# Kernel tuning notes

Measured on AMD Instinct MI355X. Metric: run time of the kernel, lower is better.

The kernel has to match this reference:

```python
import jax, jax.numpy as jnp
import numpy as np

G = 2        # num_code_vector_groups
V = 320      # num_code_vectors_per_group
D1 = 512     # extracted_feature_size
DCV = 768    # code_vector_size
DG = DCV // G  # per-group code vector dim = 384
TAU = 2.0    # gumbel_init_temperature
B, L = 16, 2048


def setup_inputs() -> dict:
    key = jax.random.key(0)
    k1, k2, k3, k4 = jax.random.split(key, 4)
    hidden_states = jax.random.normal(k1, (B, L, D1), dtype=jnp.float32)
    W = jax.random.normal(k2, (G * V, D1), dtype=jnp.float32) * 0.02
    b = jnp.zeros((G * V,), dtype=jnp.float32)
    code_book = jax.random.normal(k3, (1, G, V, DG), dtype=jnp.float32)
    # fixed Gumbel noise (torch samples it inside F.gumbel_softmax)
    gumbel_noise = jax.random.gumbel(k4, (B * L * G, V), dtype=jnp.float32)
    return {"hidden_states": hidden_states, "W": W, "b": b,
            "code_book": code_book, "gumbel_noise": gumbel_noise}


def reference(hidden_states, W, b, code_book, gumbel_noise):
    batch, length, _ = hidden_states.shape
    # linear projection: (B, L, G*V)
    logits = jnp.einsum('bld,od->blo', hidden_states, W) + b
    flat = logits.reshape(batch * length * G, V)  # (N*G, V)

    # gumbel_softmax(hard=True): straight-through hard one-hot
    y_soft = jax.nn.softmax((flat + gumbel_noise) / TAU, axis=-1)
    idx = jnp.argmax(y_soft, axis=-1)
    y_hard = jax.nn.one_hot(idx, V, dtype=y_soft.dtype)
    probs = y_hard + y_soft - jax.lax.stop_gradient(y_soft)  # (N*G, V)

    # redundant second softmax for perplexity (faithful to source)
    soft_dist = jax.nn.softmax(logits.reshape(batch, length, G, V), axis=-1)
    perplexity = soft_dist.sum(0) / batch  # (L, G, V) — sum over dim 0 only

    # code_vectors: (probs.unsqueeze(-1) * code_book).sum(-2) as an einsum
    p = probs.reshape(batch * length, G, V)
    code_vectors = jnp.einsum('ngv,gvd->ngd', p, code_book[0])
    code_vectors = code_vectors.reshape(batch, length, G * DG)  # (B, L, 768)
    return code_vectors, perplexity
```

## Files before the change

kernel.cpp:

```cpp
#include <hip/hip_runtime.h>

#define B_    16
#define L_    2048
#define D1_   512
#define G_    2
#define V_    320
#define GV_   640
#define DG_   384
#define NROW_ 32768
#define OUT0_ ((size_t)B_ * L_ * G_ * DG_)
#define WS_BYTES_ ((size_t)GV_ * D1_ * 2u)
#define WSA_OFF_SH_ ((size_t)GV_ * D1_)
#define LG_OFF_SH_  (WSA_OFF_SH_ + (size_t)NROW_ * D1_)
#define SPLIT2_WS_  ((LG_OFF_SH_ + (size_t)NROW_ * GV_) * 2u)
#define THR_  2e-2f
#define GPAD_ 324

typedef __attribute__((ext_vector_type(8))) short          s16x8;
typedef __attribute__((ext_vector_type(4))) float          f32x4;
typedef __attribute__((ext_vector_type(4))) int            s32x4;
typedef __attribute__((ext_vector_type(4))) unsigned short u16x4;

__device__ __forceinline__ unsigned short f2bf(float x) {
    unsigned u = __float_as_uint(x);
    u += 0x7fffu + ((u >> 16) & 1u);
    return (unsigned short)(u >> 16);
}
__device__ __forceinline__ float bf2f(unsigned short h) {
    return __uint_as_float(((unsigned)h) << 16);
}
__device__ __forceinline__ unsigned cvtpk(float lo, float hi) {
    unsigned r;
    asm("v_cvt_pk_bf16_f32 %0, %1, %2" : "=v"(r) : "v"(lo), "v"(hi));
    return r;
}
union PU { unsigned u[4]; s16x8 v; };
__device__ __forceinline__ s16x8 pack8(const float4& a, const float4& b) {
    PU p;
    p.u[0] = cvtpk(a.x, a.y); p.u[1] = cvtpk(a.z, a.w);
    p.u[2] = cvtpk(b.x, b.y); p.u[3] = cvtpk(b.z, b.w);
    return p.v;
}
__device__ __forceinline__ void merge2(float& m1, int& i1, float& m2, int& i2,
                                       float om1, int oi1, float om2, int oi2) {
    if (om1 > m1 || (om1 == m1 && oi1 < i1)) {
        if (m1 > om2 || (m1 == om2 && i1 < oi2)) { m2 = m1; i2 = i1; }
        else                                     { m2 = om2; i2 = oi2; }
        m1 = om1; i1 = oi1;
    } else if (om1 > m2 || (om1 == m2 && oi1 < i2)) { m2 = om1; i2 = oi1; }
}

__global__ void prep_w_kernel(const float* __restrict__ W, unsigned short* __restrict__ ws) {
    int flat = blockIdx.x * 256 + threadIdx.x;
    int o  = flat >> 7;
    int j0 = (flat & 127) << 2;
    float4 v = *(const float4*)(W + (size_t)o * D1_ + j0);
    int ch = o >> 4, kk = j0 >> 5;
    int slot = (o & 15) + (((j0 >> 3) & 3) << 4);
    size_t off = (((size_t)(ch * 16 + kk) * 64 + slot) << 3) + (j0 & 7);
    ws[off + 0] = f2bf(v.x); ws[off + 1] = f2bf(v.y);
    ws[off + 2] = f2bf(v.z); ws[off + 3] = f2bf(v.w);
}

__global__ void prep_a_kernel(const float* __restrict__ hidden, unsigned short* __restrict__ wsA) {
    size_t flat = (size_t)blockIdx.x * 256 + threadIdx.x;
    int r  = (int)(flat >> 7);
    int j0 = ((int)flat & 127) << 2;
    float4 v = *(const float4*)(hidden + ((size_t)r << 9) + j0);
    int ch = r >> 4, kk = j0 >> 5;
    int slot = (r & 15) + (((j0 >> 3) & 3) << 4);
    size_t off = (((size_t)(ch * 16 + kk) * 64 + slot) << 3) + (j0 & 7);
    wsA[off + 0] = f2bf(v.x); wsA[off + 1] = f2bf(v.y);
    wsA[off + 2] = f2bf(v.z); wsA[off + 3] = f2bf(v.w);
}

__global__ __launch_bounds__(512, 4) void k1_gemm(
    const unsigned short* __restrict__ wsW,
    const unsigned short* __restrict__ wsA,
    const float* __restrict__ bias,
    unsigned short* __restrict__ lgout)
{
    const int tid = threadIdx.x;
    const int w = tid >> 6, lane = tid & 63;
    const int rg = w >> 1, cg = w & 1;
    const int q = lane >> 4, c = lane & 15;
    const int d = blockIdx.x;
    const int mt = (d & 7) * 32 + (d >> 5);
    const int ct = (d >> 3) & 3;

    const unsigned short* a0p = wsA + ((size_t)(mt * 8 + rg * 2 + 0) << 13) + (lane << 3);
    const unsigned short* a1p = wsA + ((size_t)(mt * 8 + rg * 2 + 1) << 13) + (lane << 3);
    const unsigned short* wp  = wsW + ((size_t)(ct * 10 + cg * 5) << 13) + (lane << 3);

    f32x4 acc0[5], acc1[5];
#pragma unroll
    for (int cf = 0; cf < 5; ++cf) { acc0[cf] = (f32x4){0,0,0,0}; acc1[cf] = (f32x4){0,0,0,0}; }

    s16x8 Aa0, Aa1, Aw0, Aw1, Aw2, Aw3, Aw4;
    s16x8 Ba0, Ba1, Bw0, Bw1, Bw2, Bw3, Bw4;

#define LD(S, KK) { \
        S##a0 = *(const s16x8*)(a0p + (KK) * 512); \
        S##a1 = *(const s16x8*)(a1p + (KK) * 512); \
        S##w0 = *(const s16x8*)(wp + 0 * 8192 + (KK) * 512); \
        S##w1 = *(const s16x8*)(wp + 1 * 8192 + (KK) * 512); \
        S##w2 = *(const s16x8*)(wp + 2 * 8192 + (KK) * 512); \
        S##w3 = *(const s16x8*)(wp + 3 * 8192 + (KK) * 512); \
        S##w4 = *(const s16x8*)(wp + 4 * 8192 + (KK) * 512); }
#define MM(S) { \
        acc0[0] = __builtin_amdgcn_mfma_f32_16x16x32_bf16(S##a0, S##w0, acc0[0], 0, 0, 0); \
        acc1[0] = __builtin_amdgcn_mfma_f32_16x16x32_bf16(S##a1, S##w0, acc1[0], 0, 0, 0); \
        acc0[1] = __builtin_amdgcn_mfma_f32_16x16x32_bf16(S##a0, S##w1, acc0[1], 0, 0, 0); \
        acc1[1] = __builtin_amdgcn_mfma_f32_16x16x32_bf16(S##a1, S##w1, acc1[1], 0, 0, 0); \
        acc0[2] = __builtin_amdgcn_mfma_f32_16x16x32_bf16(S##a0, S##w2, acc0[2], 0, 0, 0); \
        acc1[2] = __builtin_amdgcn_mfma_f32_16x16x32_bf16(S##a1, S##w2, acc1[2], 0, 0, 0); \
        acc0[3] = __builtin_amdgcn_mfma_f32_16x16x32_bf16(S##a0, S##w3, acc0[3], 0, 0, 0); \
        acc1[3] = __builtin_amdgcn_mfma_f32_16x16x32_bf16(S##a1, S##w3, acc1[3], 0, 0, 0); \
        acc0[4] = __builtin_amdgcn_mfma_f32_16x16x32_bf16(S##a0, S##w4, acc0[4], 0, 0, 0); \
        acc1[4] = __builtin_amdgcn_mfma_f32_16x16x32_bf16(S##a1, S##w4, acc1[4], 0, 0, 0); }

    LD(A, 0)
#pragma unroll 1
    for (int kp = 0; kp < 8; ++kp) {
        LD(B, 2 * kp + 1)
        MM(A)
        if (kp < 7) LD(A, 2 * kp + 2)
        MM(B)
    }
#undef LD
#undef MM

    float bv[5];
#pragma unroll
    for (int cf = 0; cf < 5; ++cf) bv[cf] = bias[ct * 160 + cg * 80 + cf * 16 + c];
#pragma unroll
    for (int rf = 0; rf < 2; ++rf) {
        size_t mrow = (size_t)mt * 128 + rg * 32 + rf * 16 + q * 4;
        unsigned short* op = lgout + mrow * GV_ + ct * 160 + cg * 80 + c;
        const f32x4* ac = rf ? acc1 : acc0;
#pragma unroll
        for (int cf = 0; cf < 5; ++cf)
#pragma unroll
            for (int r = 0; r < 4; ++r)
                op[(size_t)r * GV_ + cf * 16] = f2bf(ac[cf][r] + bv[cf]);
    }
}

__global__ __launch_bounds__(256, 4) void k2_epi(
    const float* __restrict__ hidden,
    const float* __restrict__ W,
    const float* __restrict__ bias,
    const float* __restrict__ cb,
    const float* __restrict__ gn,
    const unsigned short* __restrict__ lgb,
    float* __restrict__ out)
{
    __shared__ float PERPW[4][GV_];
    const int tid = threadIdx.x;
    const int w = tid >> 6, lane = tid & 63;
    const int h = lane >> 5, k = lane & 31;
    const int l = blockIdx.x;

    f32x4 pac0 = {0,0,0,0}, pac1 = {0,0,0,0}, pac2 = {0,0,0,0};

    f32x4 Alg0, Alg1, Alg2, Agv0, Agv1, Agv2;
    f32x4 Blg0, Blg1, Blg2, Bgv0, Bgv1, Bgv2;

#define NTL(p) __builtin_nontemporal_load((const f32x4*)(p))
#define LOADROW(S, RR) { \
        size_t row_ = ((size_t)(w * 4 + (RR))) * L_ + l; \
        const unsigned short* lrb = lgb + row_ * GV_ + h * V_ + (k << 2); \
        const float* grb = gn + row_ * GV_ + h * V_ + (k << 2); \
        u16x4 L0 = *(const u16x4*)(lrb); \
        u16x4 L1 = *(const u16x4*)(lrb + 128); \
        S##gv0 = NTL(grb); S##gv1 = NTL(grb + 128); \
        _Pragma("unroll") \
        for (int j = 0; j < 4; ++j) { S##lg0[j] = bf2f(L0[j]); S##lg1[j] = bf2f(L1[j]); } \
        if (k < 16) { \
            u16x4 L2 = *(const u16x4*)(lrb + 256); \
            S##gv2 = NTL(grb + 256); \
            _Pragma("unroll") \
            for (int j = 0; j < 4; ++j) S##lg2[j] = bf2f(L2[j]); \
        } }

#define EXACT(CI, EN) { \
        if (EN) { \
            const int ci_ = (CI); \
            const float* ar_ = hidden + row_ * D1_ + (k << 4); \
            const float* wr_ = W + (size_t)(h * V_ + ci_) * D1_ + (k << 4); \
            double s_ = 0.0; \
            _Pragma("unroll 4") \
            for (int j = 0; j < 16; ++j) s_ = fma((double)ar_[j], (double)wr_[j], s_); \
            _Pragma("unroll") \
            for (int off = 1; off <= 16; off <<= 1) s_ += __shfl_xor(s_, off); \
            s_ += (double)bias[h * V_ + ci_] + (double)gn[row_ * GV_ + h * V_ + ci_]; \
            if (s_ > bestv || (s_ == bestv && ci_ < bi)) { bestv = s_; bi = ci_; } \
        } }

#define PROCROW(S, RR) { \
        const size_t row_ = ((size_t)(w * 4 + (RR))) * L_ + l; \
         \
        _Pragma("unroll") \
        for (int j = 0; j < 4; ++j) { S##gv0[j] += S##lg0[j]; S##gv1[j] += S##lg1[j]; } \
        if (k < 16) { _Pragma("unroll") for (int j = 0; j < 4; ++j) S##gv2[j] += S##lg2[j]; } \
         \
        float m1 = -3e38f; \
        _Pragma("unroll") \
        for (int j = 0; j < 4; ++j) { m1 = fmaxf(m1, S##gv0[j]); m1 = fmaxf(m1, S##gv1[j]); } \
        if (k < 16) { _Pragma("unroll") for (int j = 0; j < 4; ++j) m1 = fmaxf(m1, S##gv2[j]); } \
        _Pragma("unroll") \
        for (int mk = 1; mk <= 16; mk <<= 1) m1 = fmaxf(m1, __shfl_xor(m1, mk)); \
         \
        int li = 0x7fffffff; \
        _Pragma("unroll") \
        for (int j = 0; j < 4; ++j) { \
            if (S##gv0[j] == m1) li = min(li, (k << 2) + j); \
            if (S##gv1[j] == m1) li = min(li, ((k + 32) << 2) + j); } \
        if (k < 16) { _Pragma("unroll") for (int j = 0; j < 4; ++j) if (S##gv2[j] == m1) li = min(li, ((k + 64) << 2) + j); } \
        _Pragma("unroll") \
        for (int mk = 1; mk <= 16; mk <<= 1) li = min(li, __shfl_xor(li, mk)); \
        const int i1 = li; \
         \
        float m2 = -3e38f; \
        _Pragma("unroll") \
        for (int j = 0; j < 4; ++j) { \
            if (((k << 2) + j) != i1)        m2 = fmaxf(m2, S##gv0[j]); \
            if ((((k + 32) << 2) + j) != i1) m2 = fmaxf(m2, S##gv1[j]); } \
        if (k < 16) { _Pragma("unroll") for (int j = 0; j < 4; ++j) if ((((k + 64) << 2) + j) != i1) m2 = fmaxf(m2, S##gv2[j]); } \
        _Pragma("unroll") \
        for (int mk = 1; mk <= 16; mk <<= 1) m2 = fmaxf(m2, __shfl_xor(m2, mk)); \
         \
        float se = 0.f; \
        _Pragma("unroll") \
        for (int j = 0; j < 4; ++j) { \
            S##lg0[j] = __expf(S##lg0[j]); se += S##lg0[j]; \
            S##lg1[j] = __expf(S##lg1[j]); se += S##lg1[j]; } \
        if (k < 16) { _Pragma("unroll") for (int j = 0; j < 4; ++j) { S##lg2[j] = __expf(S##lg2[j]); se += S##lg2[j]; } } \
        _Pragma("unroll") \
        for (int mk = 1; mk <= 16; mk <<= 1) se += __shfl_xor(se, mk); \
        const float inv = 1.0f / (se * 16.0f); \
        _Pragma("unroll") \
        for (int j = 0; j < 4; ++j) { pac0[j] += S##lg0[j] * inv; pac1[j] += S##lg1[j] * inv; } \
        if (k < 16) { _Pragma("unroll") for (int j = 0; j < 4; ++j) pac2[j] += S##lg2[j] * inv; } \
        int idx = i1; \
        if (m1 - m2 < THR_) { \
             \
            int li2 = 0x7fffffff; \
            _Pragma("unroll") \
            for (int j = 0; j < 4; ++j) { \
                int v0 = (k << 2) + j;        if (v0 != i1 && S##gv0[j] == m2) li2 = min(li2, v0); \
                int v1 = ((k + 32) << 2) + j; if (v1 != i1 && S##gv1[j] == m2) li2 = min(li2, v1); } \
            if (k < 16) { _Pragma("unroll") for (int j = 0; j < 4; ++j) { int v2 = ((k + 64) << 2) + j; if (v2 != i1 && S##gv2[j] == m2) li2 = min(li2, v2); } } \
            _Pragma("unroll") \
            for (int mk = 1; mk <= 16; mk <<= 1) li2 = min(li2, __shfl_xor(li2, mk)); \
            const int i2 = li2; \
            float m3 = -3e38f; \
            _Pragma("unroll") \
            for (int j = 0; j < 4; ++j) { \
                int v0 = (k << 2) + j;        if (v0 != i1 && v0 != i2) m3 = fmaxf(m3, S##gv0[j]); \
                int v1 = ((k + 32) << 2) + j; if (v1 != i1 && v1 != i2) m3 = fmaxf(m3, S##gv1[j]); } \
            if (k < 16) { _Pragma("unroll") for (int j = 0; j < 4; ++j) { int v2 = ((k + 64) << 2) + j; if (v2 != i1 && v2 != i2) m3 = fmaxf(m3, S##gv2[j]); } } \
            _Pragma("unroll") \
            for (int mk = 1; mk <= 16; mk <<= 1) m3 = fmaxf(m3, __shfl_xor(m3, mk)); \
            int li3 = 0x7fffffff; \
            _Pragma("unroll") \
            for (int j = 0; j < 4; ++j) { \
                int v0 = (k << 2) + j;        if (v0 != i1 && v0 != i2 && S##gv0[j] == m3) li3 = min(li3, v0); \
                int v1 = ((k + 32) << 2) + j; if (v1 != i1 && v1 != i2 && S##gv1[j] == m3) li3 = min(li3, v1); } \
            if (k < 16) { _Pragma("unroll") for (int j = 0; j < 4; ++j) { int v2 = ((k + 64) << 2) + j; if (v2 != i1 && v2 != i2 && S##gv2[j] == m3) li3 = min(li3, v2); } } \
            _Pragma("unroll") \
            for (int mk = 1; mk <= 16; mk <<= 1) li3 = min(li3, __shfl_xor(li3, mk)); \
            const int i3 = li3; \
            double bestv = -1e300; int bi = 0; \
            EXACT(i1, true) \
            EXACT(i2, true) \
            EXACT(i3, (m1 - m3 < THR_)) \
            idx = bi; \
        } \
        { \
            const float* src = cb + (size_t)(h * V_ + idx) * DG_ + (k << 2); \
            float* dst = out + row_ * (G_ * DG_) + h * DG_ + (k << 2); \
            __builtin_nontemporal_store(*(const f32x4*)(src),       (f32x4*)(dst)); \
            __builtin_nontemporal_store(*(const f32x4*)(src + 128), (f32x4*)(dst + 128)); \
            __builtin_nontemporal_store(*(const f32x4*)(src + 256), (f32x4*)(dst + 256)); \
        } }

    LOADROW(A, 0)
    LOADROW(B, 1)
    PROCROW(A, 0)
    LOADROW(A, 2)
    PROCROW(B, 1)
    LOADROW(B, 3)
    PROCROW(A, 2)
    PROCROW(B, 3)
#undef NTL
#undef LOADROW
#undef EXACT
#undef PROCROW

    *(f32x4*)&PERPW[w][h * V_ + (k << 2)]        = pac0;
    *(f32x4*)&PERPW[w][h * V_ + ((k + 32) << 2)] = pac1;
    if (k < 16)
        *(f32x4*)&PERPW[w][h * V_ + ((k + 64) << 2)] = pac2;
    __syncthreads();

    if (tid < 160) {
        f32x4 s = *(const f32x4*)&PERPW[0][tid * 4];
#pragma unroll
        for (int ww = 1; ww < 4; ++ww) {
            f32x4 t = *(const f32x4*)&PERPW[ww][tid * 4];
#pragma unroll
            for (int j = 0; j < 4; ++j) s[j] += t[j];
        }
        __builtin_nontemporal_store(s, (f32x4*)(out + OUT0_ + (size_t)l * GV_ + tid * 4));
    }
}

template<bool HAS_WS>
__global__ __launch_bounds__(512, 4) void gvq7_kernel(
    const float* __restrict__ hidden,
    const float* __restrict__ W,
    const float* __restrict__ bias,
    const float* __restrict__ cb,
    const float* __restrict__ gn,
    float* __restrict__ out,
    const unsigned short* __restrict__ ws)
{
    __shared__ float GLDS[32][GPAD_];
    __shared__ __align__(16) float pm1[4][64], pm2[4][64], plx[4][64], psum[4][64];
    __shared__ __align__(16) int   pi1[4][64], pi2[4][64];
    __shared__ int IDX[64];
    __shared__ int qn, qrow[64], qc1[64], qc2[64];

    const int tid  = threadIdx.x;
    const int w    = tid >> 6, lane = tid & 63;
    const int rg   = w >> 2, cg = w & 3;
    const int q    = lane >> 4, c = lane & 15;
    const int d    = blockIdx.x;
    const int g    = (d >> 3) & 1;
    const int lq   = (d >> 4) * 8 + (d & 7);
    const size_t lbase = (size_t)lq * 4;

    if (tid == 0) qn = 0;

    const int arow = lane & 15;
    const int kq8  = (lane >> 4) * 8;
    const float* aP0 = hidden + ((size_t)arow * L_ + lbase + rg * 2) * D1_ + kq8;
    const float* aP1 = aP0 + D1_;
    const unsigned short* wP = ws + (size_t)(g * 20 + cg * 5) * 8192 + (size_t)lane * 8;
    const float* wfP = W + ((size_t)(g * V_ + cg * 80 + arow)) * D1_ + kq8;

    const int srow = tid >> 4, t16 = tid & 15;
    const float* gnst = gn + (((size_t)(srow & 15) * L_ + lbase + ((srow >> 4) << 1)) * G_ + g) * V_
                           + (t16 << 2);

    f32x4 acc0[5], acc1[5];
#pragma unroll
    for (int cf = 0; cf < 5; ++cf) { acc0[cf] = (f32x4){0,0,0,0}; acc1[cf] = (f32x4){0,0,0,0}; }

    float4 Aa0, Aa1, Aa2, Aa3, Ba0, Ba1, Ba2, Ba3;
    s16x8 Aw0, Aw1, Aw2, Aw3, Aw4, Bw0, Bw1, Bw2, Bw3, Bw4;
    s16x8 fA0, fA1, fB0, fB1;

#define LDA(S, R) { S##a0 = *(const float4*)(aP0 + (R)*32);     S##a1 = *(const float4*)(aP0 + (R)*32 + 4); \
                    S##a2 = *(const float4*)(aP1 + (R)*32);     S##a3 = *(const float4*)(aP1 + (R)*32 + 4); }
#define LDW1(S, CF, R) { if (HAS_WS) { S##w##CF = *(const s16x8*)(wP + (CF)*8192 + (R)*512); } \
                         else { float4 x_ = *(const float4*)(wfP + (CF)*8192 + (R)*32); \
                                float4 y_ = *(const float4*)(wfP + (CF)*8192 + (R)*32 + 4); \
                                S##w##CF = pack8(x_, y_); } }
#define LDW(S, R) { LDW1(S,0,R) LDW1(S,1,R) LDW1(S,2,R) LDW1(S,3,R) LDW1(S,4,R) }
#define CVT(S) { f##S##0 = pack8(S##a0, S##a1); f##S##1 = pack8(S##a2, S##a3); }
#define MM1(S, CF) { acc0[CF] = __builtin_amdgcn_mfma_f32_16x16x32_bf16(f##S##0, S##w##CF, acc0[CF], 0, 0, 0); \
                     acc1[CF] = __builtin_amdgcn_mfma_f32_16x16x32_bf16(f##S##1, S##w##CF, acc1[CF], 0, 0, 0); }
#define MM(S) { MM1(S,0) MM1(S,1) MM1(S,2) MM1(S,3) MM1(S,4) }

    LDA(A, 0) LDW(A, 0)
#pragma unroll 1
    for (int kp = 0; kp < 8; ++kp) {
        CVT(A)
        LDA(B, 1) LDW(B, 1)
        MM(A)
        CVT(B)
        if (kp < 7) { LDA(A, 2) LDW(A, 2) }
        MM(B)
        aP0 += 64; aP1 += 64; wP += 1024; wfP += 64;
    }
#undef LDA
#undef LDW1
#undef LDW
#undef CVT
#undef MM1
#undef MM

    float bv[5];
#pragma unroll
    for (int cf = 0; cf < 5; ++cf) bv[cf] = bias[g * V_ + cg * 80 + cf * 16 + c];
#pragma unroll
    for (int cf = 0; cf < 5; ++cf)
#pragma unroll
        for (int r = 0; r < 4; ++r) { acc0[cf][r] += bv[cf]; acc1[cf][r] += bv[cf]; }

    auto scanrf = [&](const f32x4* a5, int rf) {
        float m1[4], m2[4], lx[4]; int i1[4], i2[4];
#pragma unroll
        for (int r = 0; r < 4; ++r) { m1[r] = -3e38f; m2[r] = -3e38f; lx[r] = -3e38f; i1[r] = 0; i2[r] = 0; }
#pragma unroll
        for (int cf = 0; cf < 5; ++cf) {
            const int col = cg * 80 + cf * 16 + c;
#pragma unroll
            for (int r = 0; r < 4; ++r) {
                float lg = a5[cf][r];
                float s  = lg + GLDS[rg * 16 + q * 4 + r][col];
                lx[r] = fmaxf(lx[r], lg);
                if (s > m1[r])      { m2[r] = m1[r]; i2[r] = i1[r]; m1[r] = s; i1[r] = col; }
                else if (s > m2[r]) { m2[r] = s; i2[r] = col; }
            }
        }
#pragma unroll
        for (int mk = 1; mk <= 8; mk <<= 1) {
#pragma unroll
            for (int r = 0; r < 4; ++r) {
                float om1 = __shfl_xor(m1[r], mk); int oi1 = __shfl_xor(i1[r], mk);
                float om2 = __shfl_xor(m2[r], mk); int oi2 = __shfl_xor(i2[r], mk);
                lx[r] = fmaxf(lx[r], __shfl_xor(lx[r], mk));
                merge2(m1[r], i1[r], m2[r], i2[r], om1, oi1, om2, oi2);
            }
        }
        if (c == 0) {
            int row0 = rg * 32 + rf * 16 + q * 4;
            *(f32x4*)&pm1[cg][row0] = (f32x4){m1[0], m1[1], m1[2], m1[3]};
            *(s32x4*)&pi1[cg][row0] = (s32x4){i1[0], i1[1], i1[2], i1[3]};
            *(f32x4*)&pm2[cg][row0] = (f32x4){m2[0], m2[1], m2[2], m2[3]};
            *(s32x4*)&pi2[cg][row0] = (s32x4){i2[0], i2[1], i2[2], i2[3]};
            *(f32x4*)&plx[cg][row0] = (f32x4){lx[0], lx[1], lx[2], lx[3]};
        }
    };

    {
        f32x4 gr[5];
#pragma unroll
        for (int j = 0; j < 5; ++j)
            gr[j] = __builtin_nontemporal_load((const f32x4*)(gnst + j * 64));
#pragma unroll
        for (int j = 0; j < 5; ++j)
            *(f32x4*)&GLDS[srow][(t16 << 2) + j * 64] = gr[j];
        __syncthreads();
        scanrf(acc0, 0);
        __syncthreads();
    }
    {
        f32x4 gr[5];
#pragma unroll
        for (int j = 0; j < 5; ++j)
            gr[j] = __builtin_nontemporal_load((const f32x4*)(gnst + GV_ + j * 64));
#pragma unroll
        for (int j = 0; j < 5; ++j)
            *(f32x4*)&GLDS[srow][(t16 << 2) + j * 64] = gr[j];
        __syncthreads();
        scanrf(acc1, 1);
        __syncthreads();
    }

    auto softrf = [&](f32x4* a5, int rf) {
        int row0 = rg * 32 + rf * 16 + q * 4;
        float LM[4], se[4];
#pragma unroll
        for (int r = 0; r < 4; ++r) {
            LM[r] = fmaxf(fmaxf(plx[0][row0 + r], plx[1][row0 + r]),
                          fmaxf(plx[2][row0 + r], plx[3][row0 + r]));
            se[r] = 0.f;
        }
#pragma unroll
        for (int cf = 0; cf < 5; ++cf)
#pragma unroll
            for (int r = 0; r < 4; ++r) {
                float e = __expf(a5[cf][r] - LM[r]);
                a5[cf][r] = e; se[r] += e;
            }
#pragma unroll
        for (int mk = 1; mk <= 8; mk <<= 1)
#pragma unroll
            for (int r = 0; r < 4; ++r) se[r] += __shfl_xor(se[r], mk);
        if (c == 0) *(f32x4*)&psum[cg][row0] = (f32x4){se[0], se[1], se[2], se[3]};
    };
    softrf(acc0, 0);
    softrf(acc1, 1);
    __syncthreads();

    auto perprf = [&](const f32x4* a5, int rf) {
        int row0 = rg * 32 + rf * 16 + q * 4;
        float IZ[4];
#pragma unroll
        for (int r = 0; r < 4; ++r)
            IZ[r] = 1.0f / ((psum[0][row0 + r] + psum[1][row0 + r]
                           + psum[2][row0 + r] + psum[3][row0 + r]) * 16.0f);
        size_t ob = OUT0_ + (lbase + rg * 2 + rf) * GV_ + g * V_ + cg * 80 + c;
#pragma unroll
        for (int cf = 0; cf < 5; ++cf) {
            float pp = a5[cf][0] * IZ[0] + a5[cf][1] * IZ[1]
                     + a5[cf][2] * IZ[2] + a5[cf][3] * IZ[3];
            pp += __shfl_xor(pp, 16); pp += __shfl_xor(pp, 32);
            if (q == 0) __builtin_nontemporal_store(pp, &out[ob + cf * 16]);
        }
    };
    perprf(acc0, 0);
    perprf(acc1, 1);

    if (tid < 64) {
        const int row = tid;
        float M1 = pm1[0][row]; int I1 = pi1[0][row];
        float M2 = pm2[0][row]; int I2 = pi2[0][row];
#pragma unroll
        for (int c2 = 1; c2 < 4; ++c2)
            merge2(M1, I1, M2, I2, pm1[c2][row], pi1[c2][row], pm2[c2][row], pi2[c2][row]);
        if (M1 - M2 >= 8e-3f) {
            IDX[row] = I1;
        } else {
            int s = atomicAdd(&qn, 1);
            qrow[s] = row; qc1[s] = I1; qc2[s] = I2;
        }
    }
    __syncthreads();

    {
        const int nq = qn;
        for (int qi = w; qi < nq; qi += 8) {
            const int row = qrow[qi];
            const int c1 = qc1[qi], c2 = qc2[qi];
            const int b = row & 15, li = row >> 4;
            const float* ar = hidden + ((size_t)b * L_ + lbase + li) * D1_ + lane * 8;
            const float* w1 = W + (size_t)(g * V_ + c1) * D1_ + lane * 8;
            const float* w2 = W + (size_t)(g * V_ + c2) * D1_ + lane * 8;
            double s1 = 0.0, s2 = 0.0;
#pragma unroll
            for (int j = 0; j < 8; ++j) {
                double a = (double)ar[j];
                s1 = fma(a, (double)w1[j], s1);
                s2 = fma(a, (double)w2[j], s2);
            }
#pragma unroll
            for (int off = 1; off < 64; off <<= 1) {
                s1 += __shfl_xor(s1, off);
                s2 += __shfl_xor(s2, off);
            }
            if (lane == 0) {
                const size_t gb = (((size_t)b * L_ + lbase + li) * G_ + g) * V_;
                s1 += (double)bias[g * V_ + c1] + (double)gn[gb + c1];
                s2 += (double)bias[g * V_ + c2] + (double)gn[gb + c2];
                IDX[row] = (s2 > s1 || (s2 == s1 && c2 < c1)) ? c2 : c1;
            }
        }
    }
    __syncthreads();

#pragma unroll 1
    for (int it = 0; it < 12; ++it) {
        int i = tid + it * 512;
        int row = i / 96, f = i - row * 96;
        int v = IDX[row];
        int b = row & 15, li = row >> 4;
        f32x4 val = *(const f32x4*)(cb + ((size_t)(g * V_ + v) * DG_) + f * 4);
        __builtin_nontemporal_store(val,
            (f32x4*)(out + ((size_t)b * L_ + lbase + li) * (G_ * DG_) + g * DG_ + f * 4));
    }
}

extern "C" void kernel_launch(void* const* d_in, const int* in_sizes, int n_in,
                              void* d_out, int out_size, void* d_ws, size_t ws_size,
                              hipStream_t stream) {
    const float* hidden   = (const float*)d_in[0];
    const float* W        = (const float*)d_in[1];
    const float* bias     = (const float*)d_in[2];
    const float* codebook = (const float*)d_in[3];
    const float* gumbel   = (const float*)d_in[4];
    float* out = (float*)d_out;

    if (ws_size >= SPLIT2_WS_) {
        unsigned short* wsW = (unsigned short*)d_ws;
        unsigned short* wsA = wsW + WSA_OFF_SH_;
        unsigned short* lgb = wsW + LG_OFF_SH_;
        prep_w_kernel<<<320, 256, 0, stream>>>(W, wsW);
        prep_a_kernel<<<16384, 256, 0, stream>>>(hidden, wsA);
        k1_gemm<<<1024, 512, 0, stream>>>(wsW, wsA, bias, lgb);
        k2_epi<<<2048, 256, 0, stream>>>(hidden, W, bias, codebook, gumbel, lgb, out);
    } else if (ws_size >= WS_BYTES_) {
        prep_w_kernel<<<320, 256, 0, stream>>>(W, (unsigned short*)d_ws);
        gvq7_kernel<true><<<1024, 512, 0, stream>>>(hidden, W, bias, codebook, gumbel, out,
                                                    (const unsigned short*)d_ws);
    } else {
        gvq7_kernel<false><<<1024, 512, 0, stream>>>(hidden, W, bias, codebook, gumbel, out,
                                                     (const unsigned short*)d_ws);
    }
}
```

Measured before the change: 122.4 us.

## Merge prep kernels and make epilogue blocks loop over four positions

Fuses the W and hidden-state bf16 prep kernels into one launch, removing one kernel launch and its boundary. The epilogue kernel now launches 512 blocks, each handling four sequence positions. It prefetches the next position's logits and noise before the block-wide perplexity reduction, and double-buffers the shared reduction buffer so one barrier per position suffices. This cuts grid size and overlaps loads with the reduction, at the cost of fewer blocks available to hide latency.

Measured after the change: 159.2 us. +30.0%, slower.

```diff
diff --git a/kernel.cpp b/kernel.cpp
--- a/kernel.cpp
+++ b/kernel.cpp
@@ -50,28 +50,29 @@
     } else if (om1 > m2 || (om1 == m2 && oi1 < i2)) { m2 = om1; i2 = oi1; }
 }
 
-__global__ void prep_w_kernel(const float* __restrict__ W, unsigned short* __restrict__ ws) {
-    int flat = blockIdx.x * 256 + threadIdx.x;
-    int o  = flat >> 7;
-    int j0 = (flat & 127) << 2;
-    float4 v = *(const float4*)(W + (size_t)o * D1_ + j0);
-    int ch = o >> 4, kk = j0 >> 5;
-    int slot = (o & 15) + (((j0 >> 3) & 3) << 4);
-    size_t off = (((size_t)(ch * 16 + kk) * 64 + slot) << 3) + (j0 & 7);
-    ws[off + 0] = f2bf(v.x); ws[off + 1] = f2bf(v.y);
-    ws[off + 2] = f2bf(v.z); ws[off + 3] = f2bf(v.w);
-}
-
-__global__ void prep_a_kernel(const float* __restrict__ hidden, unsigned short* __restrict__ wsA) {
-    size_t flat = (size_t)blockIdx.x * 256 + threadIdx.x;
-    int r  = (int)(flat >> 7);
-    int j0 = ((int)flat & 127) << 2;
-    float4 v = *(const float4*)(hidden + ((size_t)r << 9) + j0);
-    int ch = r >> 4, kk = j0 >> 5;
-    int slot = (r & 15) + (((j0 >> 3) & 3) << 4);
-    size_t off = (((size_t)(ch * 16 + kk) * 64 + slot) << 3) + (j0 & 7);
-    wsA[off + 0] = f2bf(v.x); wsA[off + 1] = f2bf(v.y);
-    wsA[off + 2] = f2bf(v.z); wsA[off + 3] = f2bf(v.w);
+__global__ void prep_all_kernel(const float* __restrict__ W, const float* __restrict__ hidden,
+                                unsigned short* __restrict__ wsW, unsigned short* __restrict__ wsA) {
+    if (blockIdx.x < 320) {
+        int flat = blockIdx.x * 256 + threadIdx.x;
+        int o  = flat >> 7;
+        int j0 = (flat & 127) << 2;
+        float4 v = *(const float4*)(W + (size_t)o * D1_ + j0);
+        int ch = o >> 4, kk = j0 >> 5;
+        int slot = (o & 15) + (((j0 >> 3) & 3) << 4);
+        size_t off = (((size_t)(ch * 16 + kk) * 64 + slot) << 3) + (j0 & 7);
+        wsW[off + 0] = f2bf(v.x); wsW[off + 1] = f2bf(v.y);
+        wsW[off + 2] = f2bf(v.z); wsW[off + 3] = f2bf(v.w);
+    } else {
+        size_t flat = (size_t)(blockIdx.x - 320) * 256 + threadIdx.x;
+        int r  = (int)(flat >> 7);
+        int j0 = ((int)flat & 127) << 2;
+        float4 v = *(const float4*)(hidden + ((size_t)r << 9) + j0);
+        int ch = r >> 4, kk = j0 >> 5;
+        int slot = (r & 15) + (((j0 >> 3) & 3) << 4);
+        size_t off = (((size_t)(ch * 16 + kk) * 64 + slot) << 3) + (j0 & 7);
+        wsA[off + 0] = f2bf(v.x); wsA[off + 1] = f2bf(v.y);
+        wsA[off + 2] = f2bf(v.z); wsA[off + 3] = f2bf(v.w);
+    }
 }
 
 __global__ __launch_bounds__(512, 4) void k1_gemm(
@@ -155,11 +156,10 @@
     const unsigned short* __restrict__ lgb,
     float* __restrict__ out)
 {
-    __shared__ float PERPW[4][GV_];
+    __shared__ float PERPW[2][4][GV_];
     const int tid = threadIdx.x;
     const int w = tid >> 6, lane = tid & 63;
     const int h = lane >> 5, k = lane & 31;
-    const int l = blockIdx.x;
 
     f32x4 pac0 = {0,0,0,0}, pac1 = {0,0,0,0}, pac2 = {0,0,0,0};
 
@@ -167,8 +167,8 @@
     f32x4 Blg0, Blg1, Blg2, Bgv0, Bgv1, Bgv2;
 
 #define NTL(p) __builtin_nontemporal_load((const f32x4*)(p))
-#define LOADROW(S, RR) { \
-        size_t row_ = ((size_t)(w * 4 + (RR))) * L_ + l; \
+#define LOADROW(S, RR, LL) { \
+        size_t row_ = ((size_t)(w * 4 + (RR))) * L_ + (LL); \
         const unsigned short* lrb = lgb + row_ * GV_ + h * V_ + (k << 2); \
         const float* grb = gn + row_ * GV_ + h * V_ + (k << 2); \
         u16x4 L0 = *(const u16x4*)(lrb); \
@@ -197,20 +197,17 @@
             if (s_ > bestv || (s_ == bestv && ci_ < bi)) { bestv = s_; bi = ci_; } \
         } }
 
-#define PROCROW(S, RR) { \
-        const size_t row_ = ((size_t)(w * 4 + (RR))) * L_ + l; \
-         \
+#define PROCROW(S, RR, LL) { \
+        const size_t row_ = ((size_t)(w * 4 + (RR))) * L_ + (LL); \
         _Pragma("unroll") \
         for (int j = 0; j < 4; ++j) { S##gv0[j] += S##lg0[j]; S##gv1[j] += S##lg1[j]; } \
         if (k < 16) { _Pragma("unroll") for (int j = 0; j < 4; ++j) S##gv2[j] += S##lg2[j]; } \
-         \
         float m1 = -3e38f; \
         _Pragma("unroll") \
         for (int j = 0; j < 4; ++j) { m1 = fmaxf(m1, S##gv0[j]); m1 = fmaxf(m1, S##gv1[j]); } \
         if (k < 16) { _Pragma("unroll") for (int j = 0; j < 4; ++j) m1 = fmaxf(m1, S##gv2[j]); } \
         _Pragma("unroll") \
         for (int mk = 1; mk <= 16; mk <<= 1) m1 = fmaxf(m1, __shfl_xor(m1, mk)); \
-         \
         int li = 0x7fffffff; \
         _Pragma("unroll") \
         for (int j = 0; j < 4; ++j) { \
@@ -220,7 +217,6 @@
         _Pragma("unroll") \
         for (int mk = 1; mk <= 16; mk <<= 1) li = min(li, __shfl_xor(li, mk)); \
         const int i1 = li; \
-         \
         float m2 = -3e38f; \
         _Pragma("unroll") \
         for (int j = 0; j < 4; ++j) { \
@@ -229,7 +225,6 @@
         if (k < 16) { _Pragma("unroll") for (int j = 0; j < 4; ++j) if ((((k + 64) << 2) + j) != i1) m2 = fmaxf(m2, S##gv2[j]); } \
         _Pragma("unroll") \
         for (int mk = 1; mk <= 16; mk <<= 1) m2 = fmaxf(m2, __shfl_xor(m2, mk)); \
-         \
         float se = 0.f; \
         _Pragma("unroll") \
         for (int j = 0; j < 4; ++j) { \
@@ -244,7 +239,6 @@
         if (k < 16) { _Pragma("unroll") for (int j = 0; j < 4; ++j) pac2[j] += S##lg2[j] * inv; } \
         int idx = i1; \
         if (m1 - m2 < THR_) { \
-             \
             int li2 = 0x7fffffff; \
             _Pragma("unroll") \
             for (int j = 0; j < 4; ++j) { \
@@ -285,35 +279,47 @@
             __builtin_nontemporal_store(*(const f32x4*)(src + 256), (f32x4*)(dst + 256)); \
         } }
 
-    LOADROW(A, 0)
-    LOADROW(B, 1)
-    PROCROW(A, 0)
-    LOADROW(A, 2)
-    PROCROW(B, 1)
-    LOADROW(B, 3)
-    PROCROW(A, 2)
-    PROCROW(B, 3)
+    int lcur = blockIdx.x;
+    LOADROW(A, 0, lcur)
+    LOADROW(B, 1, lcur)
+#pragma unroll
+    for (int li = 0; li < 4; ++li) {
+        PROCROW(A, 0, lcur)
+        LOADROW(A, 2, lcur)
+        PROCROW(B, 1, lcur)
+        LOADROW(B, 3, lcur)
+        PROCROW(A, 2, lcur)
+        PROCROW(B, 3, lcur)
+
+        const int pb = li & 1;
+        *(f32x4*)&PERPW[pb][w][h * V_ + (k << 2)]        = pac0;
+        *(f32x4*)&PERPW[pb][w][h * V_ + ((k + 32) << 2)] = pac1;
+        if (k < 16)
+            *(f32x4*)&PERPW[pb][w][h * V_ + ((k + 64) << 2)] = pac2;
+        pac0 = (f32x4){0,0,0,0}; pac1 = (f32x4){0,0,0,0}; pac2 = (f32x4){0,0,0,0};
+
+        const int lred = lcur;
+        lcur += 512;
+        if (li < 3) {
+            LOADROW(A, 0, lcur)
+            LOADROW(B, 1, lcur)
+        }
+        __syncthreads();
+        if (tid < 160) {
+            f32x4 s = *(const f32x4*)&PERPW[pb][0][tid * 4];
+#pragma unroll
+            for (int ww = 1; ww < 4; ++ww) {
+                f32x4 t = *(const f32x4*)&PERPW[pb][ww][tid * 4];
+#pragma unroll
+                for (int j = 0; j < 4; ++j) s[j] += t[j];
+            }
+            __builtin_nontemporal_store(s, (f32x4*)(out + OUT0_ + (size_t)lred * GV_ + tid * 4));
+        }
+    }
 #undef NTL
 #undef LOADROW
 #undef EXACT
 #undef PROCROW
-
-    *(f32x4*)&PERPW[w][h * V_ + (k << 2)]        = pac0;
-    *(f32x4*)&PERPW[w][h * V_ + ((k + 32) << 2)] = pac1;
-    if (k < 16)
-        *(f32x4*)&PERPW[w][h * V_ + ((k + 64) << 2)] = pac2;
-    __syncthreads();
-
-    if (tid < 160) {
-        f32x4 s = *(const f32x4*)&PERPW[0][tid * 4];
-#pragma unroll
-        for (int ww = 1; ww < 4; ++ww) {
-            f32x4 t = *(const f32x4*)&PERPW[ww][tid * 4];
-#pragma unroll
-            for (int j = 0; j < 4; ++j) s[j] += t[j];
-        }
-        __builtin_nontemporal_store(s, (f32x4*)(out + OUT0_ + (size_t)l * GV_ + tid * 4));
-    }
 }
 
 template<bool HAS_WS>
@@ -579,12 +585,11 @@
         unsigned short* wsW = (unsigned short*)d_ws;
         unsigned short* wsA = wsW + WSA_OFF_SH_;
         unsigned short* lgb = wsW + LG_OFF_SH_;
-        prep_w_kernel<<<320, 256, 0, stream>>>(W, wsW);
-        prep_a_kernel<<<16384, 256, 0, stream>>>(hidden, wsA);
+        prep_all_kernel<<<320 + 16384, 256, 0, stream>>>(W, hidden, wsW, wsA);
         k1_gemm<<<1024, 512, 0, stream>>>(wsW, wsA, bias, lgb);
-        k2_epi<<<2048, 256, 0, stream>>>(hidden, W, bias, codebook, gumbel, lgb, out);
+        k2_epi<<<512, 256, 0, stream>>>(hidden, W, bias, codebook, gumbel, lgb, out);
     } else if (ws_size >= WS_BYTES_) {
-        prep_w_kernel<<<320, 256, 0, stream>>>(W, (unsigned short*)d_ws);
+        prep_all_kernel<<<320, 256, 0, stream>>>(W, hidden, (unsigned short*)d_ws, nullptr);
         gvq7_kernel<true><<<1024, 512, 0, stream>>>(hidden, W, bias, codebook, gumbel, out,
                                                     (const unsigned short*)d_ws);
     } else {
```
